# Optimization experiments

Measured on AMD Instinct MI355X. Metric: run time of the kernel, lower is better.

## Reference

```python
import jax, jax.numpy as jnp
import numpy as np
import math

WINDOW_SIZE = 1024
CAUSAL = True


def setup_inputs() -> dict:
    key = jax.random.key(0)
    kq, kk, kv = jax.random.split(key, 3)
    B, H, L, D = 2, 16, 4096, 128
    q = jax.random.normal(kq, (B, H, L, D), dtype=jnp.float32)
    k = jax.random.normal(kk, (B, H, L, D), dtype=jnp.float32)
    v = jax.random.normal(kv, (B, H, L, D), dtype=jnp.float32)
    return {"q": q, "k": k, "v": v}


def _sliding_window_attention(q, k, v):
    # Faithful port of SlidingWindowAttention._blockwise_attention (L > 2048 path).
    B, H, L, D = q.shape
    block = min(WINDOW_SIZE, 1024)
    scale = 1.0 / math.sqrt(D)
    half_w = WINDOW_SIZE // 2
    outs = []
    # Python loop over a small fixed number of blocks (L/block = 4), not data dims.
    for s in range(0, L, block):
        e = min(s + block, L)
        ks = max(0, s - half_w)
        ke = min(L, e + half_w)
        if CAUSAL:
            ke = min(ke, e)
        qb = q[:, :, s:e, :]          # [B,H,Q,D]
        kb = k[:, :, ks:ke, :]        # [B,H,K,D]
        vb = v[:, :, ks:ke, :]        # [B,H,K,D]
        scores = jnp.einsum('bhqd,bhkd->bhqk', qb, kb) * scale
        if CAUSAL:
            qi = jnp.arange(s, e)[:, None]   # [Q,1]
            ki = jnp.arange(ks, ke)[None, :]  # [1,K]
            causal_mask = qi >= ki            # [Q,K]
            scores = jnp.where(causal_mask[None, None], scores, -jnp.inf)
        attn = jax.nn.softmax(scores, axis=-1)
        outs.append(jnp.einsum('bhqk,bhkd->bhqd', attn, vb))
    return jnp.concatenate(outs, axis=2)


def reference(q, k, v):
    return _sliding_window_attention(q, k, v)
```

## Files before the change

### kernel.cpp

```cpp
#include <hip/hip_runtime.h>
#include <hip/hip_bf16.h>
#include <stdint.h>

typedef __bf16 bf16_t;
typedef __bf16 bf16x8 __attribute__((ext_vector_type(8)));
typedef __bf16 bf16x4 __attribute__((ext_vector_type(4)));
typedef float f32x4 __attribute__((ext_vector_type(4)));

#define L_SEQ 4096
#define D_DIM 128
#define NBH   32
#define KT    32
#define LDP   36

__global__ __launch_bounds__(256)
void cvt_kv(const float* __restrict__ Kg, const float* __restrict__ Vg,
            bf16_t* __restrict__ Kws, bf16_t* __restrict__ Vws) {
    const int b = blockIdx.x;
    if (b < 8192) {
        const int n   = b * 256 + threadIdx.x;
        const int key = n >> 4;
        const int pc  = n & 15;
        const int lc  = pc ^ (key & 7);
        const float* s = Kg + (size_t)key * D_DIM + lc * 8;
        f32x4 a = *(const f32x4*)(s);
        f32x4 c = *(const f32x4*)(s + 4);
        bf16x8 h;
        #pragma unroll
        for (int j = 0; j < 4; ++j) { h[j] = (bf16_t)a[j]; h[4 + j] = (bf16_t)c[j]; }
        *(bf16x8*)(Kws + (size_t)key * D_DIM + pc * 8) = h;
    } else {
        const int blk  = b - 8192;
        const int bh   = blk >> 7;
        const int kb   = blk & 127;
        const int t    = threadIdx.x;
        const int d    = t & 127;
        const int half = t >> 7;
        const float* src0 = Vg + (size_t)(bh * L_SEQ + kb * 32) * D_DIM + d;
        bf16_t* dstrow = Vws + ((size_t)(bh * 128 + kb) * D_DIM + d) * 32;
        const int sw = (d >> 1) & 3;
        #pragma unroll
        for (int r2 = 0; r2 < 2; ++r2) {
            const int lc = half + 2 * r2;
            bf16x8 h;
            #pragma unroll
            for (int j = 0; j < 8; ++j)
                h[j] = (bf16_t)src0[(size_t)(lc * 8 + j) * D_DIM];
            *(bf16x8*)(&dstrow[(lc ^ sw) * 8]) = h;
        }
    }
}

__device__ __forceinline__ void ld_lds16(const void* g, void* s) {
    __builtin_amdgcn_global_load_lds(
        (const __attribute__((address_space(1))) unsigned int*)g,
        (__attribute__((address_space(3))) unsigned int*)s, 16, 0, 0);
}

#define QT2 128

__global__ __launch_bounds__(256, 3)
void swa_fwd4(const float* __restrict__ Qg,
              const bf16_t* __restrict__ Kws,
              const bf16_t* __restrict__ Vws,
              float* __restrict__ Og) {
    __shared__ __align__(16) bf16_t KtS[3][KT * D_DIM];
    __shared__ __align__(16) bf16_t VtS[3][D_DIM * KT];
    __shared__ __align__(16) bf16_t Pst[4][16 * LDP];

    const int t    = threadIdx.x;
    const int w    = t >> 6;
    const int ln   = t & 15;
    const int quad = (t & 63) >> 4;
    const int l7   = t & 7;

    const int id = blockIdx.x;
    const int bh = id & 31;
    const int g  = id >> 5;
    const int r_ = g & 7;
    const int k_ = g >> 3;
    const int qt = 8 * k_ + ((k_ & 1) ? (7 - r_) : r_);

    const size_t baseF = (size_t)bh * L_SEQ * D_DIM;
    const float*  Qp = Qg + baseF;
    float*        Op = Og + baseF;
    const bf16_t* Kb = Kws + baseF;
    const bf16_t* Vb = Vws + (size_t)bh * 128 * D_DIM * 32;

    const int qbase  = qt * QT2;
    const int blk    = qbase & ~1023;
    const int kstart = (blk - 512) > 0 ? (blk - 512) : 0;
    const int kend   = qbase + QT2;
    const int ntile  = (kend - kstart) / KT;

    const int qw    = qbase + w * 32;
    const int qwmax = qw + 31;

    const float SC  = 0.08838834764831845f * 1.4426950408889634f;
    const float FIX = 8.0f;
    const float NEG = -1.0e30f;

    bf16x8 qf[2][4];
    #pragma unroll
    for (int mt = 0; mt < 2; ++mt) {
        const float* qrow = Qp + (size_t)(qw + mt * 16 + ln) * D_DIM + quad * 8;
        #pragma unroll
        for (int ks = 0; ks < 4; ++ks) {
            f32x4 a = *(const f32x4*)(qrow + ks * 32);
            f32x4 b = *(const f32x4*)(qrow + ks * 32 + 4);
            bf16x8 q8;
            #pragma unroll
            for (int j = 0; j < 4; ++j) { q8[j] = (bf16_t)(a[j] * SC); q8[4 + j] = (bf16_t)(b[j] * SC); }
            qf[mt][ks] = q8;
        }
    }

    f32x4 Oacc[2][8];
    #pragma unroll
    for (int mt = 0; mt < 2; ++mt)
        #pragma unroll
        for (int dt = 0; dt < 8; ++dt) Oacc[mt][dt] = f32x4{0.f, 0.f, 0.f, 0.f};
    float lsum[2] = {0.f, 0.f};

    auto stage = [&](bf16_t* kd_, bf16_t* vd_, int k0) {
        const char* ksrc = (const char*)Kb + (size_t)k0 * 256;
        const char* vsrc = (const char*)Vb + (size_t)(k0 >> 5) * 8192;
        #pragma unroll
        for (int i = 0; i < 2; ++i) {
            const int off = (i * 256 + t) * 16;
            ld_lds16(ksrc + off, (char*)kd_ + off);
            ld_lds16(vsrc + off, (char*)vd_ + off);
        }
    };

    bf16_t *kc = &KtS[0][0], *kn = &KtS[1][0], *kf = &KtS[2][0];
    bf16_t *vc = &VtS[0][0], *vn = &VtS[1][0], *vf = &VtS[2][0];

    stage(kc, vc, kstart);
    stage(kn, vn, kstart + KT);
    asm volatile("s_waitcnt vmcnt(4)" ::: "memory");
    __builtin_amdgcn_s_barrier();
    __builtin_amdgcn_sched_barrier(0);

    for (int n = 0; n < ntile; ++n) {
        const int k0 = kstart + n * KT;
        if (n + 2 < ntile) stage(kf, vf, k0 + 2 * KT);

        if (k0 <= qwmax) {
            f32x4 S[2][2];
            #pragma unroll
            for (int mt = 0; mt < 2; ++mt)
                #pragma unroll
                for (int nt = 0; nt < 2; ++nt) S[mt][nt] = f32x4{0.f, 0.f, 0.f, 0.f};
            __builtin_amdgcn_s_setprio(1);
            #pragma unroll
            for (int ks = 0; ks < 4; ++ks) {
                #pragma unroll
                for (int nt = 0; nt < 2; ++nt) {
                    const bf16x8 bk = *(const bf16x8*)(
                        &kc[(nt * 16 + ln) * D_DIM + (((ks * 4 + quad) ^ l7) * 8)]);
                    S[0][nt] = __builtin_amdgcn_mfma_f32_16x16x32_bf16(bk, qf[0][ks], S[0][nt], 0, 0, 0);
                    S[1][nt] = __builtin_amdgcn_mfma_f32_16x16x32_bf16(bk, qf[1][ks], S[1][nt], 0, 0, 0);
                }
            }
            __builtin_amdgcn_s_setprio(0);

            bf16x8 pa[2];
            #pragma unroll
            for (int mt = 0; mt < 2; ++mt) {
                const int qwm = qw + mt * 16;
                const int qg  = qwm + ln;
                const bool nm = (k0 + KT - 1) > qwm;
                #pragma unroll
                for (int nt = 0; nt < 2; ++nt) {
                    bf16x4 hp;
                    #pragma unroll
                    for (int r = 0; r < 4; ++r) {
                        float s = S[mt][nt][r];
                        if (nm) {
                            const int kg = k0 + nt * 16 + quad * 4 + r;
                            if (kg > qg) s = NEG;
                        }
                        const float e = __builtin_amdgcn_exp2f(s - FIX);
                        lsum[mt] += e;
                        hp[r] = (bf16_t)e;
                    }
                    *(bf16x4*)(&Pst[w][ln * LDP + (nt * 2 + (quad >> 1)) * 8 + (quad & 1) * 4]) = hp;
                }
                pa[mt] = *(const bf16x8*)(&Pst[w][ln * LDP + quad * 8]);
            }

            __builtin_amdgcn_s_setprio(1);
            #pragma unroll
            for (int dt = 0; dt < 8; ++dt) {
                const bf16x8 bv = *(const bf16x8*)(
                    &vc[(dt * 16 + ln) * KT + ((quad ^ ((ln >> 1) & 3)) * 8)]);
                Oacc[0][dt] = __builtin_amdgcn_mfma_f32_16x16x32_bf16(bv, pa[0], Oacc[0][dt], 0, 0, 0);
                Oacc[1][dt] = __builtin_amdgcn_mfma_f32_16x16x32_bf16(bv, pa[1], Oacc[1][dt], 0, 0, 0);
            }
            __builtin_amdgcn_s_setprio(0);
        }

        if (n + 1 < ntile) {
            if (n + 2 < ntile) {
                asm volatile("s_waitcnt vmcnt(4)" ::: "memory");
            } else {
                asm volatile("s_waitcnt vmcnt(0)" ::: "memory");
            }
            __builtin_amdgcn_s_barrier();
            __builtin_amdgcn_sched_barrier(0);
        }

        bf16_t* tk = kc; kc = kn; kn = kf; kf = tk;
        bf16_t* tv = vc; vc = vn; vn = vf; vf = tv;
    }

    #pragma unroll
    for (int mt = 0; mt < 2; ++mt) {
        float l = lsum[mt];
        l += __shfl_xor(l, 16, 64);
        l += __shfl_xor(l, 32, 64);
        const float inv = (l > 0.f) ? (1.f / l) : 0.f;
        const int qg = qw + mt * 16 + ln;
        float* orow = Op + (size_t)qg * D_DIM + quad * 4;
        #pragma unroll
        for (int dt = 0; dt < 8; ++dt) {
            f32x4 o = Oacc[mt][dt];
            #pragma unroll
            for (int j = 0; j < 4; ++j) o[j] *= inv;
            *(f32x4*)(orow + dt * 16) = o;
        }
    }
}

#define QTF 64
#define KTF 64
#define LDK 136
#define LDV 72
#define LDPF 72

__global__ __launch_bounds__(256, 2)
void swa_fwd(const float* __restrict__ Qg,
             const float* __restrict__ Kg,
             const float* __restrict__ Vg,
             float* __restrict__ Og) {
    __shared__ __align__(16) bf16_t Kt[KTF][LDK];
    __shared__ __align__(16) bf16_t Vt[D_DIM][LDV];
    __shared__ __align__(16) bf16_t Pstf[4][16][LDPF];

    const int t    = threadIdx.x;
    const int w    = t >> 6;
    const int ln   = t & 15;
    const int quad = (t & 63) >> 4;

    const int id = blockIdx.x;
    const int bh = id & 31;
    const int g  = id >> 5;
    const int q0 = g & 7;
    const int kk = g >> 3;
    const int qt = 16 * (kk >> 1) + ((kk & 1) ? (15 - q0) : q0);

    const size_t base = (size_t)bh * L_SEQ * D_DIM;
    const float* Qp = Qg + base;
    const float* Kp = Kg + base;
    const float* Vp = Vg + base;
    float*       Op = Og + base;

    const int qbase  = qt * QTF;
    const int blk    = qbase & ~1023;
    const int kstart = (blk - 512) > 0 ? (blk - 512) : 0;
    const int kend   = qbase + QTF;
    const int ntile  = (kend - kstart) / KTF;

    const int qw = qbase + w * 16;

    const float SC  = 0.08838834764831845f * 1.4426950408889634f;
    const float FIX = 8.0f;

    bf16x8 qf[4];
    {
        const float* qrow = Qp + (size_t)(qw + ln) * D_DIM + quad * 8;
        #pragma unroll
        for (int ks = 0; ks < 4; ++ks) {
            f32x4 a = *(const f32x4*)(qrow + ks * 32);
            f32x4 b = *(const f32x4*)(qrow + ks * 32 + 4);
            bf16x8 q8;
            #pragma unroll
            for (int j = 0; j < 4; ++j) {
                q8[j]     = (bf16_t)(a[j] * SC);
                q8[4 + j] = (bf16_t)(b[j] * SC);
            }
            qf[ks] = q8;
        }
    }

    f32x4 Oacc[8];
    #pragma unroll
    for (int dt = 0; dt < 8; ++dt) Oacc[dt] = f32x4{0.f, 0.f, 0.f, 0.f};
    float lsum[4] = {0.f, 0.f, 0.f, 0.f};
    const float NEG = -1.0e30f;

    const int kr   = t >> 5;
    const int kc   = t & 31;
    const int vd   = t & 127;
    const int vkcb = t >> 7;

    f32x4 kreg[8];
    float vreg[4][8];

    auto load_tile = [&](int k0) {
        #pragma unroll
        for (int i = 0; i < 8; ++i)
            kreg[i] = *(const f32x4*)(Kp + (size_t)(k0 + kr + 8 * i) * D_DIM + kc * 4);
        #pragma unroll
        for (int r2 = 0; r2 < 4; ++r2) {
            const int kcc = vkcb + 2 * r2;
            #pragma unroll
            for (int j = 0; j < 8; ++j)
                vreg[r2][j] = Vp[(size_t)(k0 + kcc * 8 + j) * D_DIM + vd];
        }
    };
    auto store_tile = [&]() {
        #pragma unroll
        for (int i = 0; i < 8; ++i) {
            bf16x4 h;
            #pragma unroll
            for (int j = 0; j < 4; ++j) h[j] = (bf16_t)kreg[i][j];
            *(bf16x4*)(&Kt[kr + 8 * i][kc * 4]) = h;
        }
        #pragma unroll
        for (int r2 = 0; r2 < 4; ++r2) {
            const int kcc = vkcb + 2 * r2;
            bf16x8 h8;
            #pragma unroll
            for (int j = 0; j < 8; ++j) h8[j] = (bf16_t)vreg[r2][j];
            *(bf16x8*)(&Vt[vd][kcc * 8]) = h8;
        }
    };

    load_tile(kstart);

    for (int kt = 0; kt < ntile; ++kt) {
        const int k0 = kstart + kt * KTF;
        __syncthreads();
        store_tile();
        __syncthreads();
        if (kt + 1 < ntile) load_tile(k0 + KTF);

        f32x4 S[4];
        #pragma unroll
        for (int nt = 0; nt < 4; ++nt) S[nt] = f32x4{0.f, 0.f, 0.f, 0.f};
        #pragma unroll
        for (int ks = 0; ks < 4; ++ks) {
            #pragma unroll
            for (int nt = 0; nt < 4; ++nt) {
                bf16x8 bk = *(const bf16x8*)(&Kt[nt * 16 + ln][quad * 8 + ks * 32]);
                S[nt] = __builtin_amdgcn_mfma_f32_16x16x32_bf16(qf[ks], bk, S[nt], 0, 0, 0);
            }
        }

        const bool lastTile = (kt == ntile - 1);
        float p[4][4];
        #pragma unroll
        for (int nt = 0; nt < 4; ++nt) {
            #pragma unroll
            for (int r = 0; r < 4; ++r) {
                float s = S[nt][r];
                if (lastTile) {
                    const int kg = k0 + nt * 16 + ln;
                    const int qg = qw + quad * 4 + r;
                    if (kg > qg) s = NEG;
                }
                const float e = __builtin_amdgcn_exp2f(s - FIX);
                p[nt][r] = e;
                lsum[r] += e;
            }
        }

        #pragma unroll
        for (int nt = 0; nt < 4; ++nt)
            #pragma unroll
            for (int r = 0; r < 4; ++r)
                Pstf[w][quad * 4 + r][nt * 16 + ln] = (bf16_t)p[nt][r];

        bf16x8 pa[2];
        #pragma unroll
        for (int ks2 = 0; ks2 < 2; ++ks2)
            pa[ks2] = *(const bf16x8*)(&Pstf[w][ln][quad * 8 + ks2 * 32]);

        #pragma unroll
        for (int dt = 0; dt < 8; ++dt) {
            #pragma unroll
            for (int ks2 = 0; ks2 < 2; ++ks2) {
                bf16x8 bv = *(const bf16x8*)(&Vt[dt * 16 + ln][quad * 8 + ks2 * 32]);
                Oacc[dt] = __builtin_amdgcn_mfma_f32_16x16x32_bf16(pa[ks2], bv, Oacc[dt], 0, 0, 0);
            }
        }
    }

    #pragma unroll
    for (int r = 0; r < 4; ++r) {
        float l = lsum[r];
        #pragma unroll
        for (int msk = 1; msk < 16; msk <<= 1)
            l += __shfl_xor(l, msk, 64);
        const float inv = (l > 0.f) ? (1.f / l) : 0.f;
        const int qg = qw + quad * 4 + r;
        float* orow = Op + (size_t)qg * D_DIM + ln;
        #pragma unroll
        for (int dt = 0; dt < 8; ++dt)
            orow[dt * 16] = Oacc[dt][r] * inv;
    }
}

extern "C" void kernel_launch(void* const* d_in, const int* in_sizes, int n_in,
                              void* d_out, int out_size, void* d_ws, size_t ws_size,
                              hipStream_t stream) {
    const float* q = (const float*)d_in[0];
    const float* k = (const float*)d_in[1];
    const float* v = (const float*)d_in[2];
    float* o = (float*)d_out;

    const size_t kbytes = (size_t)NBH * L_SEQ * D_DIM * sizeof(bf16_t);
    if (d_ws && ws_size >= 2 * kbytes) {
        bf16_t* kws = (bf16_t*)d_ws;
        bf16_t* vws = (bf16_t*)((char*)d_ws + kbytes);
        cvt_kv<<<dim3(12288), dim3(256), 0, stream>>>(k, v, kws, vws);
        swa_fwd4<<<dim3(1024), dim3(256), 0, stream>>>(q, kws, vws, o);
    } else {
        swa_fwd<<<dim3(2048), dim3(256), 0, stream>>>(q, k, v, o);
    }
}
```

Measured before the change: 279.1 us.

## Switch attention kernel to 32x32x16 MFMA with permlane32 P-transpose and new K/V layout

Replaces the 16x16x32 MFMA tiling with 32x32x16 bf16 MFMAs, so each wave handles its 32 query rows as one tile. The softmax probabilities are repacked across lanes with permlane32_swap instead of going through an LDS scratch buffer, which removes those LDS round trips. The K/V conversion kernel is rewritten so both tensors are stored in per-32-key blocked fragment layouts that match the new MFMA operand loads. The risks are LDS bank conflicts from dropping the XOR swizzle and different register pressure with the 16-wide accumulators.

New measurement: 278.1 us. No clear change (-0.4%).

```diff
diff --git a/kernel.cpp b/kernel.cpp
--- a/kernel.cpp
+++ b/kernel.cpp
@@ -5,48 +5,52 @@
 typedef __bf16 bf16_t;
 typedef __bf16 bf16x8 __attribute__((ext_vector_type(8)));
 typedef __bf16 bf16x4 __attribute__((ext_vector_type(4)));
+typedef __bf16 bf16x2 __attribute__((ext_vector_type(2)));
 typedef float f32x4 __attribute__((ext_vector_type(4)));
+typedef float f32x16 __attribute__((ext_vector_type(16)));
+typedef unsigned int u32x4 __attribute__((ext_vector_type(4)));
 
 #define L_SEQ 4096
 #define D_DIM 128
 #define NBH   32
 #define KT    32
-#define LDP   36
 
 __global__ __launch_bounds__(256)
 void cvt_kv(const float* __restrict__ Kg, const float* __restrict__ Vg,
             bf16_t* __restrict__ Kws, bf16_t* __restrict__ Vws) {
     const int b = blockIdx.x;
-    if (b < 8192) {
-        const int n   = b * 256 + threadIdx.x;
-        const int key = n >> 4;
-        const int pc  = n & 15;
-        const int lc  = pc ^ (key & 7);
-        const float* s = Kg + (size_t)key * D_DIM + lc * 8;
-        f32x4 a = *(const f32x4*)(s);
-        f32x4 c = *(const f32x4*)(s + 4);
-        bf16x8 h;
-        #pragma unroll
-        for (int j = 0; j < 4; ++j) { h[j] = (bf16_t)a[j]; h[4 + j] = (bf16_t)c[j]; }
-        *(bf16x8*)(Kws + (size_t)key * D_DIM + pc * 8) = h;
+    const int t = threadIdx.x;
+    if (b < 4096) {
+        const int bh = b >> 7, kb = b & 127;
+        const int key = t >> 3, part = t & 7;
+        const float* src = Kg + (size_t)(bh * L_SEQ + kb * 32 + key) * D_DIM + part * 16;
+        bf16_t* out = Kws + (size_t)(bh * 128 + kb) * 4096;
+        f32x4 a0 = *(const f32x4*)(src);
+        f32x4 a1 = *(const f32x4*)(src + 4);
+        f32x4 a2 = *(const f32x4*)(src + 8);
+        f32x4 a3 = *(const f32x4*)(src + 12);
+        bf16x8 h0, h1;
+        #pragma unroll
+        for (int j = 0; j < 4; ++j) {
+            h0[j] = (bf16_t)a0[j]; h0[4 + j] = (bf16_t)a1[j];
+            h1[j] = (bf16_t)a2[j]; h1[4 + j] = (bf16_t)a3[j];
+        }
+        *(bf16x8*)(out + ((part * 2)     * 32 + key) * 8) = h0;
+        *(bf16x8*)(out + ((part * 2 + 1) * 32 + key) * 8) = h1;
     } else {
-        const int blk  = b - 8192;
-        const int bh   = blk >> 7;
-        const int kb   = blk & 127;
-        const int t    = threadIdx.x;
-        const int d    = t & 127;
-        const int half = t >> 7;
+        const int blk = b - 4096;
+        const int bh = blk >> 7, kb = blk & 127;
+        const int d = t & 127, half = t >> 7;
         const float* src0 = Vg + (size_t)(bh * L_SEQ + kb * 32) * D_DIM + d;
-        bf16_t* dstrow = Vws + ((size_t)(bh * 128 + kb) * D_DIM + d) * 32;
-        const int sw = (d >> 1) & 3;
+        bf16_t* out = Vws + (size_t)(bh * 128 + kb) * 4096;
         #pragma unroll
         for (int r2 = 0; r2 < 2; ++r2) {
-            const int lc = half + 2 * r2;
+            const int kc = half * 2 + r2;
             bf16x8 h;
             #pragma unroll
             for (int j = 0; j < 8; ++j)
-                h[j] = (bf16_t)src0[(size_t)(lc * 8 + j) * D_DIM];
-            *(bf16x8*)(&dstrow[(lc ^ sw) * 8]) = h;
+                h[j] = (bf16_t)src0[(size_t)(kc * 8 + j) * D_DIM];
+            *(bf16x8*)(out + kc * 1024 + d * 8) = h;
         }
     }
 }
@@ -57,22 +61,23 @@
         (__attribute__((address_space(3))) unsigned int*)s, 16, 0, 0);
 }
 
-#define QT2 128
+__device__ __forceinline__ unsigned pkbf(float a, float b) {
+    bf16x2 h; h[0] = (bf16_t)a; h[1] = (bf16_t)b;
+    return __builtin_bit_cast(unsigned, h);
+}
 
 __global__ __launch_bounds__(256, 3)
-void swa_fwd4(const float* __restrict__ Qg,
+void swa_fwd5(const float* __restrict__ Qg,
               const bf16_t* __restrict__ Kws,
               const bf16_t* __restrict__ Vws,
               float* __restrict__ Og) {
-    __shared__ __align__(16) bf16_t KtS[3][KT * D_DIM];
-    __shared__ __align__(16) bf16_t VtS[3][D_DIM * KT];
-    __shared__ __align__(16) bf16_t Pst[4][16 * LDP];
-
-    const int t    = threadIdx.x;
-    const int w    = t >> 6;
-    const int ln   = t & 15;
-    const int quad = (t & 63) >> 4;
-    const int l7   = t & 7;
+    __shared__ __align__(16) bf16_t KtS[3][4096];
+    __shared__ __align__(16) bf16_t VtS[3][4096];
+
+    const int t   = threadIdx.x;
+    const int w   = t >> 6;
+    const int l31 = t & 31;
+    const int hi  = (t >> 5) & 1;
 
     const int id = blockIdx.x;
     const int bh = id & 31;
@@ -85,45 +90,44 @@
     const float*  Qp = Qg + baseF;
     float*        Op = Og + baseF;
     const bf16_t* Kb = Kws + baseF;
-    const bf16_t* Vb = Vws + (size_t)bh * 128 * D_DIM * 32;
-
-    const int qbase  = qt * QT2;
+    const bf16_t* Vb = Vws + baseF;
+
+    const int qbase  = qt * 128;
     const int blk    = qbase & ~1023;
     const int kstart = (blk - 512) > 0 ? (blk - 512) : 0;
-    const int kend   = qbase + QT2;
+    const int kend   = qbase + 128;
     const int ntile  = (kend - kstart) / KT;
 
-    const int qw    = qbase + w * 32;
-    const int qwmax = qw + 31;
+    const int qw = qbase + w * 32;
+    const int qg = qw + l31;
 
     const float SC  = 0.08838834764831845f * 1.4426950408889634f;
     const float FIX = 8.0f;
     const float NEG = -1.0e30f;
 
-    bf16x8 qf[2][4];
+    bf16x8 qf[8];
+    {
+        const float* qrow = Qp + (size_t)qg * D_DIM + hi * 8;
+        #pragma unroll
+        for (int ko = 0; ko < 8; ++ko) {
+            f32x4 a = *(const f32x4*)(qrow + ko * 16);
+            f32x4 b = *(const f32x4*)(qrow + ko * 16 + 4);
+            bf16x8 q8;
+            #pragma unroll
+            for (int j = 0; j < 4; ++j) { q8[j] = (bf16_t)(a[j] * SC); q8[4 + j] = (bf16_t)(b[j] * SC); }
+            qf[ko] = q8;
+        }
+    }
+
+    f32x16 Oacc[4];
     #pragma unroll
-    for (int mt = 0; mt < 2; ++mt) {
-        const float* qrow = Qp + (size_t)(qw + mt * 16 + ln) * D_DIM + quad * 8;
-        #pragma unroll
-        for (int ks = 0; ks < 4; ++ks) {
-            f32x4 a = *(const f32x4*)(qrow + ks * 32);
-            f32x4 b = *(const f32x4*)(qrow + ks * 32 + 4);
-            bf16x8 q8;
-            #pragma unroll
-            for (int j = 0; j < 4; ++j) { q8[j] = (bf16_t)(a[j] * SC); q8[4 + j] = (bf16_t)(b[j] * SC); }
-            qf[mt][ks] = q8;
-        }
-    }
-
-    f32x4 Oacc[2][8];
-    #pragma unroll
-    for (int mt = 0; mt < 2; ++mt)
-        #pragma unroll
-        for (int dt = 0; dt < 8; ++dt) Oacc[mt][dt] = f32x4{0.f, 0.f, 0.f, 0.f};
-    float lsum[2] = {0.f, 0.f};
+    for (int dt = 0; dt < 4; ++dt)
+        #pragma unroll
+        for (int i = 0; i < 16; ++i) Oacc[dt][i] = 0.f;
+    float lsum = 0.f;
 
     auto stage = [&](bf16_t* kd_, bf16_t* vd_, int k0) {
-        const char* ksrc = (const char*)Kb + (size_t)k0 * 256;
+        const char* ksrc = (const char*)Kb + (size_t)(k0 >> 5) * 8192;
         const char* vsrc = (const char*)Vb + (size_t)(k0 >> 5) * 8192;
         #pragma unroll
         for (int i = 0; i < 2; ++i) {
@@ -146,57 +150,55 @@
         const int k0 = kstart + n * KT;
         if (n + 2 < ntile) stage(kf, vf, k0 + 2 * KT);
 
-        if (k0 <= qwmax) {
-            f32x4 S[2][2];
-            #pragma unroll
-            for (int mt = 0; mt < 2; ++mt)
+        if (k0 <= qw + 31) {
+            const char* kbase = (const char*)kc + (hi * 512 + l31 * 16);
+            f32x16 S;
+            #pragma unroll
+            for (int i = 0; i < 16; ++i) S[i] = 0.f;
+            __builtin_amdgcn_s_setprio(1);
+            #pragma unroll
+            for (int ko = 0; ko < 8; ++ko) {
+                const bf16x8 kfrg = *(const bf16x8*)(kbase + ko * 1024);
+                S = __builtin_amdgcn_mfma_f32_32x32x16_bf16(kfrg, qf[ko], S, 0, 0, 0);
+            }
+            __builtin_amdgcn_s_setprio(0);
+
+            const bool nm = (k0 + KT - 1) > qw;
+            bf16x8 pb0, pb1;
+            #pragma unroll
+            for (int tt = 0; tt < 2; ++tt) {
+                float e[8];
                 #pragma unroll
-                for (int nt = 0; nt < 2; ++nt) S[mt][nt] = f32x4{0.f, 0.f, 0.f, 0.f};
+                for (int rr = 0; rr < 8; ++rr) {
+                    float s = S[tt * 8 + rr];
+                    if (nm) {
+                        const int kg = k0 + tt * 16 + (rr & 3) + 8 * (rr >> 2) + 4 * hi;
+                        if (kg > qg) s = NEG;
+                    }
+                    const float ev = __builtin_amdgcn_exp2f(s - FIX);
+                    lsum += ev;
+                    e[rr] = ev;
+                }
+                unsigned P0 = pkbf(e[0], e[1]);
+                unsigned P1 = pkbf(e[2], e[3]);
+                unsigned P2 = pkbf(e[4], e[5]);
+                unsigned P3 = pkbf(e[6], e[7]);
+                auto r02 = __builtin_amdgcn_permlane32_swap(P0, P2, false, false);
+                auto r13 = __builtin_amdgcn_permlane32_swap(P1, P3, false, false);
+                u32x4 pw;
+                pw[0] = r02[0]; pw[1] = r13[0]; pw[2] = r02[1]; pw[3] = r13[1];
+                if (tt == 0) pb0 = __builtin_bit_cast(bf16x8, pw);
+                else         pb1 = __builtin_bit_cast(bf16x8, pw);
+            }
+
+            const char* vbase = (const char*)vc + (hi * 2048 + l31 * 16);
             __builtin_amdgcn_s_setprio(1);
             #pragma unroll
-            for (int ks = 0; ks < 4; ++ks) {
-                #pragma unroll
-                for (int nt = 0; nt < 2; ++nt) {
-                    const bf16x8 bk = *(const bf16x8*)(
-                        &kc[(nt * 16 + ln) * D_DIM + (((ks * 4 + quad) ^ l7) * 8)]);
-                    S[0][nt] = __builtin_amdgcn_mfma_f32_16x16x32_bf16(bk, qf[0][ks], S[0][nt], 0, 0, 0);
-                    S[1][nt] = __builtin_amdgcn_mfma_f32_16x16x32_bf16(bk, qf[1][ks], S[1][nt], 0, 0, 0);
-                }
-            }
-            __builtin_amdgcn_s_setprio(0);
-
-            bf16x8 pa[2];
-            #pragma unroll
-            for (int mt = 0; mt < 2; ++mt) {
-                const int qwm = qw + mt * 16;
-                const int qg  = qwm + ln;
-                const bool nm = (k0 + KT - 1) > qwm;
-                #pragma unroll
-                for (int nt = 0; nt < 2; ++nt) {
-                    bf16x4 hp;
-                    #pragma unroll
-                    for (int r = 0; r < 4; ++r) {
-                        float s = S[mt][nt][r];
-                        if (nm) {
-                            const int kg = k0 + nt * 16 + quad * 4 + r;
-                            if (kg > qg) s = NEG;
-                        }
-                        const float e = __builtin_amdgcn_exp2f(s - FIX);
-                        lsum[mt] += e;
-                        hp[r] = (bf16_t)e;
-                    }
-                    *(bf16x4*)(&Pst[w][ln * LDP + (nt * 2 + (quad >> 1)) * 8 + (quad & 1) * 4]) = hp;
-                }
-                pa[mt] = *(const bf16x8*)(&Pst[w][ln * LDP + quad * 8]);
-            }
-
-            __builtin_amdgcn_s_setprio(1);
-            #pragma unroll
-            for (int dt = 0; dt < 8; ++dt) {
-                const bf16x8 bv = *(const bf16x8*)(
-                    &vc[(dt * 16 + ln) * KT + ((quad ^ ((ln >> 1) & 3)) * 8)]);
-                Oacc[0][dt] = __builtin_amdgcn_mfma_f32_16x16x32_bf16(bv, pa[0], Oacc[0][dt], 0, 0, 0);
-                Oacc[1][dt] = __builtin_amdgcn_mfma_f32_16x16x32_bf16(bv, pa[1], Oacc[1][dt], 0, 0, 0);
+            for (int dt = 0; dt < 4; ++dt) {
+                const bf16x8 v0 = *(const bf16x8*)(vbase + dt * 512);
+                Oacc[dt] = __builtin_amdgcn_mfma_f32_32x32x16_bf16(v0, pb0, Oacc[dt], 0, 0, 0);
+                const bf16x8 v1 = *(const bf16x8*)(vbase + 4096 + dt * 512);
+                Oacc[dt] = __builtin_amdgcn_mfma_f32_32x32x16_bf16(v1, pb1, Oacc[dt], 0, 0, 0);
             }
             __builtin_amdgcn_s_setprio(0);
         }
@@ -215,20 +217,17 @@
         bf16_t* tv = vc; vc = vn; vn = vf; vf = tv;
     }
 
+    float l = lsum + __shfl_xor(lsum, 32, 64);
+    const float inv = (l > 0.f) ? (1.f / l) : 0.f;
+    float* orow = Op + (size_t)qg * D_DIM;
     #pragma unroll
-    for (int mt = 0; mt < 2; ++mt) {
-        float l = lsum[mt];
-        l += __shfl_xor(l, 16, 64);
-        l += __shfl_xor(l, 32, 64);
-        const float inv = (l > 0.f) ? (1.f / l) : 0.f;
-        const int qg = qw + mt * 16 + ln;
-        float* orow = Op + (size_t)qg * D_DIM + quad * 4;
-        #pragma unroll
-        for (int dt = 0; dt < 8; ++dt) {
-            f32x4 o = Oacc[mt][dt];
-            #pragma unroll
-            for (int j = 0; j < 4; ++j) o[j] *= inv;
-            *(f32x4*)(orow + dt * 16) = o;
+    for (int dt = 0; dt < 4; ++dt) {
+        #pragma unroll
+        for (int g2 = 0; g2 < 4; ++g2) {
+            f32x4 o;
+            #pragma unroll
+            for (int j = 0; j < 4; ++j) o[j] = Oacc[dt][g2 * 4 + j] * inv;
+            *(f32x4*)(orow + dt * 32 + g2 * 8 + hi * 4) = o;
         }
     }
 }
@@ -425,8 +424,8 @@
     if (d_ws && ws_size >= 2 * kbytes) {
         bf16_t* kws = (bf16_t*)d_ws;
         bf16_t* vws = (bf16_t*)((char*)d_ws + kbytes);
-        cvt_kv<<<dim3(12288), dim3(256), 0, stream>>>(k, v, kws, vws);
-        swa_fwd4<<<dim3(1024), dim3(256), 0, stream>>>(q, kws, vws, o);
+        cvt_kv<<<dim3(8192), dim3(256), 0, stream>>>(k, v, kws, vws);
+        swa_fwd5<<<dim3(1024), dim3(256), 0, stream>>>(q, kws, vws, o);
     } else {
         swa_fwd<<<dim3(2048), dim3(256), 0, stream>>>(q, k, v, o);
     }
```
